# Performance work log

Hardware: AMD Instinct MI355X
Metric: run time of the kernel (lower is better)

The kernel has to match this reference:

```python
import jax, jax.numpy as jnp
import numpy as np

E = 512   # decoder embedding dim
H = 2048  # decoder hidden size


def setup_inputs() -> dict:
    key = jax.random.key(0)
    ks = jax.random.split(key, 10)
    V, B, T, S = 50000, 32, 128, 128
    s = 0.05
    return {
        "embed_table": jax.random.normal(ks[0], (V, E), jnp.float32) * s,
        "encoder_outs": jax.random.normal(ks[1], (S, B, 2 * 512), jnp.float32),
        "encoder_hiddens": jax.random.normal(ks[2], (1, B, H), jnp.float32) * s,
        "encoder_cells": jax.random.normal(ks[3], (1, B, H), jnp.float32) * s,
        "W_ih": jax.random.normal(ks[4], (4 * H, 2048), jnp.float32) * s,
        "W_hh": jax.random.normal(ks[5], (4 * H, H), jnp.float32) * s,
        "b_ih": jax.random.normal(ks[6], (4 * H,), jnp.float32) * s,
        "b_hh": jax.random.normal(ks[7], (4 * H,), jnp.float32) * s,
        "prev_output_tokens": jax.random.randint(ks[8], (B, T), 0, V),
        "tgt_langs": jax.random.randint(ks[9], (B,), 0, V),
    }


def reference(embed_table, encoder_outs, encoder_hiddens, encoder_cells,
              W_ih, W_hh, b_ih, b_hh, prev_output_tokens, tgt_langs):
    # bottleneck: max-pool encoder states over source time (LASER-style)
    context = jnp.max(encoder_outs, axis=0)                 # [B, 2*enc_hidden]
    x = embed_table[prev_output_tokens]                      # [B, T, E]
    x = jnp.transpose(x, (1, 0, 2))                          # [T, B, E]
    lang_embed = embed_table[tgt_langs]                      # [B, E]

    # Per-step LSTM input is concat(x_t, lang, context). lang/context are
    # time-invariant, so precompute their gate contribution once.
    static_in = jnp.concatenate([lang_embed, context], axis=1)   # [B, E + 2*enc]
    gates_x = (jnp.einsum('tbe,ge->tbg', x, W_ih[:, :E])
               + static_in @ W_ih[:, E:].T + b_ih + b_hh)        # [T, B, 4H]

    h0 = encoder_hiddens[0]
    c0 = encoder_cells[0]

    def step(carry, g_x):
        h, c = carry
        gates = g_x + h @ W_hh.T                              # [B, 4H]
        i, f, g, o = jnp.split(gates, 4, axis=1)
        c = jax.nn.sigmoid(f) * c + jax.nn.sigmoid(i) * jnp.tanh(g)
        h = jax.nn.sigmoid(o) * jnp.tanh(c)
        return (h, c), h

    _, outs = jax.lax.scan(step, (h0, c0), gates_x)           # [T, B, H]
    return outs
```

## Files before the change

kernel.cpp:

```cpp
#include <hip/hip_runtime.h>
#include <math.h>

#define E_DIM 512
#define H_DIM 2048
#define G_DIM 8192
#define B_DIM 32
#define T_DIM 128
#define S_DIM 128
#define ENC2  1024
#define SI_DIM 1536

#define NBLK 256
#define NTHR 512
#define JT   8
#define KHW  (H_DIM/8)
#define KXW  (E_DIM/8)
#define HB   (B_DIM*H_DIM)
#define HPLANE 65536



typedef __bf16 bf16_t;
typedef bf16_t bf16x8 __attribute__((ext_vector_type(8)));
typedef float f32x4 __attribute__((ext_vector_type(4)));
typedef unsigned int u32x4 __attribute__((ext_vector_type(4)));

__device__ __forceinline__ unsigned short f2bf(float x) {
    unsigned u = __float_as_uint(x);
    u += 0x7FFFu + ((u >> 16) & 1u);
    return (unsigned short)(u >> 16);
}
__device__ __forceinline__ float bf2f(unsigned short s) {
    return __uint_as_float(((unsigned)s) << 16);
}
__device__ __forceinline__ unsigned pack2(float a, float b) {
    return (unsigned)f2bf(a) | ((unsigned)f2bf(b) << 16);
}
__device__ __forceinline__ f32x4 mfma16(bf16x8 a, bf16x8 b, f32x4 c) {
    return __builtin_amdgcn_mfma_f32_16x16x32_bf16(a, b, c, 0, 0, 0);
}
__device__ __forceinline__ bf16x8 tofrag(u32x4 q) {
    return __builtin_bit_cast(bf16x8, q);
}
__device__ __forceinline__ float sigf(float x) { return 1.f / (1.f + expf(-x)); }

#define OPAQUE(v) asm volatile("" : "+v"(v))
#define ALD(p) __hip_atomic_load((p), __ATOMIC_RELAXED, __HIP_MEMORY_SCOPE_AGENT)

struct WPair { u32x4 hi, lo; };
__device__ __forceinline__ WPair packW(const float* src) {
    float4 w0 = *(const float4*)src;
    float4 w1 = *(const float4*)(src + 16);
    u32x4 qh;
    qh.x = pack2(w0.x, w0.y); qh.y = pack2(w0.z, w0.w);
    qh.z = pack2(w1.x, w1.y); qh.w = pack2(w1.z, w1.w);
    float r0 = w0.x - bf2f((unsigned short)(qh.x & 0xFFFF));
    float r1 = w0.y - bf2f((unsigned short)(qh.x >> 16));
    float r2 = w0.z - bf2f((unsigned short)(qh.y & 0xFFFF));
    float r3 = w0.w - bf2f((unsigned short)(qh.y >> 16));
    float r4 = w1.x - bf2f((unsigned short)(qh.z & 0xFFFF));
    float r5 = w1.y - bf2f((unsigned short)(qh.z >> 16));
    float r6 = w1.z - bf2f((unsigned short)(qh.w & 0xFFFF));
    float r7 = w1.w - bf2f((unsigned short)(qh.w >> 16));
    u32x4 ql;
    ql.x = pack2(r0, r1); ql.y = pack2(r2, r3);
    ql.z = pack2(r4, r5); ql.w = pack2(r6, r7);
    WPair out; out.hi = qh; out.lo = ql;
    return out;
}

__global__ void k_prep(const float* __restrict__ enc_outs, const float* __restrict__ embed,
                       const int* __restrict__ langs, const float* __restrict__ h0,
                       float* __restrict__ si, unsigned short* __restrict__ hth,
                       unsigned short* __restrict__ htl, unsigned int* __restrict__ flags) {
    int tid = blockIdx.x * blockDim.x + threadIdx.x;
    int np = gridDim.x * blockDim.x;
    for (int i = tid; i < NBLK * 16; i += np)
        flags[i] = 0u;
    for (int i = tid; i < B_DIM * ENC2; i += np) {
        int b = i >> 10, e = i & 1023;
        float m = -3.4e38f;
        for (int s = 0; s < S_DIM; ++s)
            m = fmaxf(m, enc_outs[(s * B_DIM + b) * ENC2 + e]);
        si[b * SI_DIM + E_DIM + e] = m;
    }
    for (int i = tid; i < B_DIM * E_DIM; i += np) {
        int b = i >> 9, e = i & 511;
        si[b * SI_DIM + e] = embed[(long)langs[b] * E_DIM + e];
    }
    for (int i = tid; i < B_DIM * H_DIM; i += np) {
        int b = i >> 11, j = i & 2047;
        float h = h0[i];
        unsigned short hi = f2bf(h);
        unsigned short lo = f2bf(h - bf2f(hi));
        int T = j >> 5, lgp = (j & 15) >> 2, o = (j & 3) + 4 * ((j & 31) >> 4);
        int idx = ((T * 4 + lgp) * 32 + b) * 8 + o;
        hth[idx] = hi;
        htl[idx] = lo;
    }
}

__global__ void k_gather_x(const float* __restrict__ embed, const int* __restrict__ tok,
                           unsigned short* __restrict__ xh, unsigned short* __restrict__ xl) {
    int r = blockIdx.x;
    int t = r >> 5, b = r & 31;
    long row = tok[b * T_DIM + t];
    const float4* src = (const float4*)(embed + row * E_DIM);
    unsigned* xhp = (unsigned*)(xh + (size_t)t * 16384);
    unsigned* xlp = (unsigned*)(xl + (size_t)t * 16384);
    for (int g = threadIdx.x; g < 128; g += blockDim.x) {
        float4 v = src[g];
        unsigned h01 = pack2(v.x, v.y), h23 = pack2(v.z, v.w);
        float rx = v.x - bf2f((unsigned short)(h01 & 0xFFFF));
        float ry = v.y - bf2f((unsigned short)(h01 >> 16));
        float rz = v.z - bf2f((unsigned short)(h23 & 0xFFFF));
        float rw = v.w - bf2f((unsigned short)(h23 >> 16));
        int T = g >> 3, lgp = g & 3, o0 = 4 * ((g & 7) >> 2);
        int u32i = ((T * 4 + lgp) * 32 + b) * 4 + (o0 >> 1);
        uint2 qh; qh.x = h01; qh.y = h23;
        uint2 ql; ql.x = pack2(rx, ry); ql.y = pack2(rz, rw);
        *(uint2*)(xhp + u32i) = qh;
        *(uint2*)(xlp + u32i) = ql;
    }
}

#define MFMA12(PH, PL, IT) \
    acc00 = mfma16(Ah0, tofrag(PH##0##IT), acc00); \
    acc00 = mfma16(Ah0, tofrag(PL##0##IT), acc00); \
    acc00 = mfma16(Al0, tofrag(PH##0##IT), acc00); \
    acc01 = mfma16(Ah1, tofrag(PH##0##IT), acc01); \
    acc01 = mfma16(Ah1, tofrag(PL##0##IT), acc01); \
    acc01 = mfma16(Al1, tofrag(PH##0##IT), acc01); \
    acc10 = mfma16(Ah0, tofrag(PH##1##IT), acc10); \
    acc10 = mfma16(Ah0, tofrag(PL##1##IT), acc10); \
    acc10 = mfma16(Al0, tofrag(PH##1##IT), acc10); \
    acc11 = mfma16(Ah1, tofrag(PH##1##IT), acc11); \
    acc11 = mfma16(Ah1, tofrag(PL##1##IT), acc11); \
    acc11 = mfma16(Al1, tofrag(PH##1##IT), acc11);

#define AX_IT(IT) do { \
    const int fb = ((wv * 2 + (IT)) * 4 + lg) * 32 + lr; \
    bf16x8 Ah0 = __builtin_bit_cast(bf16x8, xh4[fb]); \
    bf16x8 Ah1 = __builtin_bit_cast(bf16x8, xh4[fb + 16]); \
    bf16x8 Al0 = __builtin_bit_cast(bf16x8, xl4[fb]); \
    bf16x8 Al1 = __builtin_bit_cast(bf16x8, xl4[fb + 16]); \
    MFMA12(Xh, Xl, IT) \
} while (0)

#define AH_IT(IT) do { \
    const int fb = ((wv * 8 + (IT)) * 4 + lg) * 32 + lr; \
    bf16x8 Ah0 = __builtin_bit_cast(bf16x8, hh4[fb]); \
    bf16x8 Ah1 = __builtin_bit_cast(bf16x8, hh4[fb + 16]); \
    bf16x8 Al0 = __builtin_bit_cast(bf16x8, hl4[fb]); \
    bf16x8 Al1 = __builtin_bit_cast(bf16x8, hl4[fb + 16]); \
    MFMA12(Wh, Wl, IT) \
} while (0)

#define PK_HH(F, IT) { WPair p = packW(W_hh + (long)rowf##F * H_DIM + (wv * KHW + IT * 32 + 4 * lg)); \
                       Wh##F##IT = p.hi; Wl##F##IT = p.lo; }
#define PK_X(F, IT)  { WPair p = packW(W_ih + (long)rowf##F * 2048 + (wv * KXW + IT * 32 + 4 * lg)); \
                       Xh##F##IT = p.hi; Xl##F##IT = p.lo; }

__global__ __launch_bounds__(NTHR, 2) void k_lstm(
        const unsigned short* __restrict__ xh, const unsigned short* __restrict__ xl,
        unsigned short* __restrict__ hth, unsigned short* __restrict__ htl,
        const float* __restrict__ si, const float* __restrict__ W_ih,
        const float* __restrict__ W_hh, const float* __restrict__ b_ih,
        const float* __restrict__ b_hh, const float* __restrict__ c0,
        float* __restrict__ out, unsigned int* __restrict__ flags) {
    __shared__ f32x4 red[8][2][2][64];
    __shared__ float gbuf[4][B_DIM][JT];
    __shared__ float sgl[4][B_DIM][JT];

    const int tid = threadIdx.x;
    const int wv = tid >> 6, l = tid & 63, lr = l & 15, lg = l >> 4;
    const int jb = blockIdx.x * JT;

    {
        int c = tid >> 4, bp = tid & 15;
        int gate = c >> 3, jl = c & 7;
        long grow = (long)(gate * H_DIM + jb + jl);
        const float* wrow = W_ih + grow * 2048 + E_DIM;
        const float* s0 = si + bp * SI_DIM;
        const float* s1 = si + (bp + 16) * SI_DIM;
        float a0 = 0.f, a1 = 0.f;
        for (int k = 0; k < SI_DIM; k += 4) {
            float4 w  = *(const float4*)(wrow + k);
            float4 x0 = *(const float4*)(s0 + k);
            float4 x1 = *(const float4*)(s1 + k);
            a0 += w.x * x0.x + w.y * x0.y + w.z * x0.z + w.w * x0.w;
            a1 += w.x * x1.x + w.y * x1.y + w.z * x1.z + w.w * x1.w;
        }
        float bias = b_ih[grow] + b_hh[grow];
        sgl[gate][bp][jl] = a0 + bias;
        sgl[gate][bp + 16][jl] = a1 + bias;
    }

    const int rowf0 = ((lr >> 3)) * H_DIM + jb + (lr & 7);
    const int rowf1 = (2 + (lr >> 3)) * H_DIM + jb + (lr & 7);

    u32x4 Wh00, Wh01, Wh02, Wh03, Wh04, Wh05, Wh06, Wh07;
    u32x4 Wh10, Wh11, Wh12, Wh13, Wh14, Wh15, Wh16, Wh17;
    u32x4 Wl00, Wl01, Wl02, Wl03, Wl04, Wl05, Wl06, Wl07;
    u32x4 Wl10, Wl11, Wl12, Wl13, Wl14, Wl15, Wl16, Wl17;
    u32x4 Xh00, Xh01, Xh10, Xh11, Xl00, Xl01, Xl10, Xl11;

    PK_HH(0, 0) PK_HH(0, 1) PK_HH(0, 2) PK_HH(0, 3)
    PK_HH(0, 4) PK_HH(0, 5) PK_HH(0, 6) PK_HH(0, 7)
    PK_HH(1, 0) PK_HH(1, 1) PK_HH(1, 2) PK_HH(1, 3)
    PK_HH(1, 4) PK_HH(1, 5) PK_HH(1, 6) PK_HH(1, 7)
    PK_X(0, 0) PK_X(0, 1) PK_X(1, 0) PK_X(1, 1)

    OPAQUE(Wh00); OPAQUE(Wh01); OPAQUE(Wh02); OPAQUE(Wh03);
    OPAQUE(Wh04); OPAQUE(Wh05); OPAQUE(Wh06); OPAQUE(Wh07);
    OPAQUE(Wh10); OPAQUE(Wh11); OPAQUE(Wh12); OPAQUE(Wh13);
    OPAQUE(Wh14); OPAQUE(Wh15); OPAQUE(Wh16); OPAQUE(Wh17);
    OPAQUE(Wl00); OPAQUE(Wl01); OPAQUE(Wl02); OPAQUE(Wl03);
    OPAQUE(Wl04); OPAQUE(Wl05); OPAQUE(Wl06); OPAQUE(Wl07);
    OPAQUE(Wl10); OPAQUE(Wl11); OPAQUE(Wl12); OPAQUE(Wl13);
    OPAQUE(Wl14); OPAQUE(Wl15); OPAQUE(Wl16); OPAQUE(Wl17);
    OPAQUE(Xh00); OPAQUE(Xh01); OPAQUE(Xh10); OPAQUE(Xh11);
    OPAQUE(Xl00); OPAQUE(Xl01); OPAQUE(Xl10); OPAQUE(Xl11);

    const int ab = (tid & 127) >> 2, ajp = (tid & 3) * 2;
    float creg0 = 0.f, creg1 = 0.f;
    if (tid < 128) {
        creg0 = c0[ab * H_DIM + jb + ajp];
        creg1 = c0[ab * H_DIM + jb + ajp + 1];
    }

    __syncthreads();

    #pragma unroll 1
    for (int t = 0; t < T_DIM; ++t) {
        f32x4 acc00 = {}, acc01 = {}, acc10 = {}, acc11 = {};

        {
            const uint4* xh4 = (const uint4*)(xh + (size_t)t * 16384);
            const uint4* xl4 = (const uint4*)(xl + (size_t)t * 16384);
            AX_IT(0); AX_IT(1);
        }

        if (t > 0) {
            const unsigned tgt = (unsigned)t;
            const bool mine = (l < 32);
            const unsigned int* fp = flags + (size_t)(wv * 32 + (l & 31)) * 16;
            for (;;) {
                unsigned v = mine ? ALD(fp) : tgt;
                if (__all(v >= tgt)) break;
                __builtin_amdgcn_s_sleep(1);
            }
            __builtin_amdgcn_sched_barrier(0);
        }

        {
            const uint4* hh4 = (const uint4*)(hth + (size_t)t * HPLANE);
            const uint4* hl4 = (const uint4*)(htl + (size_t)t * HPLANE);
            AH_IT(0); AH_IT(1); AH_IT(2); AH_IT(3);
            AH_IT(4); AH_IT(5); AH_IT(6); AH_IT(7);
        }

        red[wv][0][0][l] = acc00; red[wv][0][1][l] = acc01;
        red[wv][1][0][l] = acc10; red[wv][1][1][l] = acc11;
        __syncthreads();
        #pragma unroll
        for (int o = tid; o < 1024; o += NTHR) {
            int f = o >> 9, m = (o >> 8) & 1, l2 = (o >> 2) & 63, r = o & 3;
            float s = 0.f;
            #pragma unroll
            for (int w = 0; w < 8; ++w) s += red[w][f][m][l2][r];
            int b = 16 * m + 4 * (l2 >> 4) + r;
            int c = l2 & 15;
            int gate = 2 * f + (c >> 3), jl = c & 7;
            gbuf[gate][b][jl] = s + sgl[gate][b][jl];
        }
        __syncthreads();

        if (tid < 128) {
            unsigned* hthn = (unsigned*)(hth + (size_t)(t + 1) * HPLANE);
            unsigned* htln = (unsigned*)(htl + (size_t)(t + 1) * HPLANE);
            float iv0 = gbuf[0][ab][ajp],     fv0 = gbuf[1][ab][ajp];
            float gv0 = gbuf[2][ab][ajp],     ov0 = gbuf[3][ab][ajp];
            float iv1 = gbuf[0][ab][ajp + 1], fv1 = gbuf[1][ab][ajp + 1];
            float gv1 = gbuf[2][ab][ajp + 1], ov1 = gbuf[3][ab][ajp + 1];
            float cn0 = sigf(fv0) * creg0 + sigf(iv0) * tanhf(gv0);
            float cn1 = sigf(fv1) * creg1 + sigf(iv1) * tanhf(gv1);
            float hn0 = sigf(ov0) * tanhf(cn0);
            float hn1 = sigf(ov1) * tanhf(cn1);
            creg0 = cn0; creg1 = cn1;
            int j0 = jb + ajp;
            unsigned short h0h = f2bf(hn0), h1h = f2bf(hn1);
            unsigned short h0l = f2bf(hn0 - bf2f(h0h));
            unsigned short h1l = f2bf(hn1 - bf2f(h1h));
            int T = j0 >> 5, lgp = (j0 & 15) >> 2, o = (j0 & 3) + 4 * ((j0 & 31) >> 4);
            int u32i = ((T * 4 + lgp) * 32 + ab) * 4 + (o >> 1);
            __hip_atomic_store(hthn + u32i, (unsigned)h0h | ((unsigned)h1h << 16),
                               __ATOMIC_RELAXED, __HIP_MEMORY_SCOPE_AGENT);
            __hip_atomic_store(htln + u32i, (unsigned)h0l | ((unsigned)h1l << 16),
                               __ATOMIC_RELAXED, __HIP_MEMORY_SCOPE_AGENT);
            float2 o2; o2.x = hn0; o2.y = hn1;
            *(float2*)(out + (size_t)t * HB + ab * H_DIM + j0) = o2;
        }

        if (t < T_DIM - 1) {
            asm volatile("s_waitcnt vmcnt(0)" ::: "memory");
            __syncthreads();
            if (tid == 0)
                __hip_atomic_store(flags + (size_t)blockIdx.x * 16,
                                   (unsigned)(t + 1), __ATOMIC_RELAXED,
                                   __HIP_MEMORY_SCOPE_AGENT);
        }
    }
}

extern "C" void kernel_launch(void* const* d_in, const int* in_sizes, int n_in,
                              void* d_out, int out_size, void* d_ws, size_t ws_size,
                              hipStream_t stream) {
    const float* embed    = (const float*)d_in[0];
    const float* enc_outs = (const float*)d_in[1];
    const float* h0       = (const float*)d_in[2];
    const float* c0       = (const float*)d_in[3];
    const float* W_ih     = (const float*)d_in[4];
    const float* W_hh     = (const float*)d_in[5];
    const float* b_ih     = (const float*)d_in[6];
    const float* b_hh     = (const float*)d_in[7];
    const int*   tok      = (const int*)d_in[8];
    const int*   langs    = (const int*)d_in[9];
    float* out = (float*)d_out;

    char* ws = (char*)d_ws;
    unsigned short* xh  = (unsigned short*)(ws + 0);
    unsigned short* xl  = (unsigned short*)(ws + 4194304);
    unsigned short* hth = (unsigned short*)(ws + 8388608);
    unsigned short* htl = (unsigned short*)(ws + 25296896);
    float*          si  = (float*)(ws + 42205184);
    unsigned int* flags = (unsigned int*)(ws + 42401792);

    hipLaunchKernelGGL(k_prep, dim3(512), dim3(256), 0, stream,
                       enc_outs, embed, langs, h0, si, hth, htl, flags);
    hipLaunchKernelGGL(k_gather_x, dim3(T_DIM * B_DIM), dim3(128), 0, stream,
                       embed, tok, xh, xl);
    hipLaunchKernelGGL(k_lstm, dim3(NBLK), dim3(NTHR), 0, stream,
                       xh, xl, hth, htl, si, W_ih, W_hh, b_ih, b_hh, c0,
                       out, flags);
}
```

Before: 1.028 ms.

## Per-wave readiness flags and fused gate reduction into pointwise threads

Result: slower. 1.330 ms (+29.3%).

```diff
diff --git a/kernel.cpp b/kernel.cpp
--- a/kernel.cpp
+++ b/kernel.cpp
@@ -169,7 +169,6 @@
         const float* __restrict__ b_hh, const float* __restrict__ c0,
         float* __restrict__ out, unsigned int* __restrict__ flags) {
     __shared__ f32x4 red[8][2][2][64];
-    __shared__ float gbuf[4][B_DIM][JT];
     __shared__ float sgl[4][B_DIM][JT];
 
     const int tid = threadIdx.x;
@@ -243,10 +242,10 @@
 
         if (t > 0) {
             const unsigned tgt = (unsigned)t;
-            const bool mine = (l < 32);
-            const unsigned int* fp = flags + (size_t)(wv * 32 + (l & 31)) * 16;
+            const unsigned int* fp =
+                flags + (size_t)(wv * 32 + (l & 31)) * 16 + (l >> 5);
             for (;;) {
-                unsigned v = mine ? ALD(fp) : tgt;
+                unsigned v = ALD(fp);
                 if (__all(v >= tgt)) break;
                 __builtin_amdgcn_s_sleep(1);
             }
@@ -263,30 +262,33 @@
         red[wv][0][0][l] = acc00; red[wv][0][1][l] = acc01;
         red[wv][1][0][l] = acc10; red[wv][1][1][l] = acc11;
         __syncthreads();
-        #pragma unroll
-        for (int o = tid; o < 1024; o += NTHR) {
-            int f = o >> 9, m = (o >> 8) & 1, l2 = (o >> 2) & 63, r = o & 3;
-            float s = 0.f;
+
+        float gs[2][4];
+        if (tid < 128) {
+            const int m = ab >> 4, r = ab & 3, bg = (ab & 15) >> 2;
             #pragma unroll
-            for (int w = 0; w < 8; ++w) s += red[w][f][m][l2][r];
-            int b = 16 * m + 4 * (l2 >> 4) + r;
-            int c = l2 & 15;
-            int gate = 2 * f + (c >> 3), jl = c & 7;
-            gbuf[gate][b][jl] = s + sgl[gate][b][jl];
+            for (int dj = 0; dj < 2; ++dj) {
+                #pragma unroll
+                for (int g = 0; g < 4; ++g) {
+                    int jl = ajp + dj;
+                    int l2 = bg * 16 + (g & 1) * 8 + jl;
+                    float s = 0.f;
+                    #pragma unroll
+                    for (int w = 0; w < 8; ++w)
+                        s += red[w][g >> 1][m][l2][r];
+                    gs[dj][g] = s + sgl[g][ab][jl];
+                }
+            }
         }
         __syncthreads();
 
         if (tid < 128) {
             unsigned* hthn = (unsigned*)(hth + (size_t)(t + 1) * HPLANE);
             unsigned* htln = (unsigned*)(htl + (size_t)(t + 1) * HPLANE);
-            float iv0 = gbuf[0][ab][ajp],     fv0 = gbuf[1][ab][ajp];
-            float gv0 = gbuf[2][ab][ajp],     ov0 = gbuf[3][ab][ajp];
-            float iv1 = gbuf[0][ab][ajp + 1], fv1 = gbuf[1][ab][ajp + 1];
-            float gv1 = gbuf[2][ab][ajp + 1], ov1 = gbuf[3][ab][ajp + 1];
-            float cn0 = sigf(fv0) * creg0 + sigf(iv0) * tanhf(gv0);
-            float cn1 = sigf(fv1) * creg1 + sigf(iv1) * tanhf(gv1);
-            float hn0 = sigf(ov0) * tanhf(cn0);
-            float hn1 = sigf(ov1) * tanhf(cn1);
+            float cn0 = sigf(gs[0][1]) * creg0 + sigf(gs[0][0]) * tanhf(gs[0][2]);
+            float cn1 = sigf(gs[1][1]) * creg1 + sigf(gs[1][0]) * tanhf(gs[1][2]);
+            float hn0 = sigf(gs[0][3]) * tanhf(cn0);
+            float hn1 = sigf(gs[1][3]) * tanhf(cn1);
             creg0 = cn0; creg1 = cn1;
             int j0 = jb + ajp;
             unsigned short h0h = f2bf(hn0), h1h = f2bf(hn1);
@@ -298,17 +300,13 @@
                                __ATOMIC_RELAXED, __HIP_MEMORY_SCOPE_AGENT);
             __hip_atomic_store(htln + u32i, (unsigned)h0l | ((unsigned)h1l << 16),
                                __ATOMIC_RELAXED, __HIP_MEMORY_SCOPE_AGENT);
+            asm volatile("s_waitcnt vmcnt(0)" ::: "memory");
+            if (l == 0 && t < T_DIM - 1)
+                __hip_atomic_store(flags + (size_t)blockIdx.x * 16 + wv,
+                                   (unsigned)(t + 1), __ATOMIC_RELAXED,
+                                   __HIP_MEMORY_SCOPE_AGENT);
             float2 o2; o2.x = hn0; o2.y = hn1;
             *(float2*)(out + (size_t)t * HB + ab * H_DIM + j0) = o2;
-        }
-
-        if (t < T_DIM - 1) {
-            asm volatile("s_waitcnt vmcnt(0)" ::: "memory");
-            __syncthreads();
-            if (tid == 0)
-                __hip_atomic_store(flags + (size_t)blockIdx.x * 16,
-                                   (unsigned)(t + 1), __ATOMIC_RELAXED,
-                                   __HIP_MEMORY_SCOPE_AGENT);
         }
     }
 }
```
